# Kernel optimization log

Hardware: AMD Instinct MI355X
Metric: run time of the kernel (lower is better)

## Reference

```python
import jax, jax.numpy as jnp
import numpy as np

B, F, U, V, C = 2048, 128, 1024, 512, 10

def setup_inputs() -> dict:
    key = jax.random.key(0)
    ks = jax.random.split(key, 8)
    s = lambda k, shape, fan: jax.random.normal(k, shape, dtype=jnp.float32) / np.sqrt(fan)
    return {
        "x": jax.random.normal(ks[0], (B, F), dtype=jnp.float32),
        # ExU first layer per feature: input dim 1 -> U units; weight stored pre-exp
        "exu_w": jax.random.normal(ks[1], (F, U), dtype=jnp.float32) * 0.5 + 4.0,
        "exu_b": jax.random.normal(ks[2], (F,), dtype=jnp.float32) * 0.5,
        # hidden dense per feature: U -> V
        "W1": s(ks[3], (F, U, V), U),
        "b1": jnp.zeros((F, V), dtype=jnp.float32),
        # output dense per feature: V -> C
        "W2": s(ks[4], (F, V, C), V),
        "b2": jnp.zeros((F, C), dtype=jnp.float32),
        # global bias over classes
        "b_out": jnp.zeros((C,), dtype=jnp.float32),
    }

def reference(x, exu_w, exu_b, W1, b1, W2, b2, b_out):
    # ExU unit: h = ReLU-1((x - b) * exp(w)); vectorized over all features at once
    # x: [B,F], exu_w/exu_b: [F,U]/[F] -> h: [B,F,U]
    h = jnp.clip((x - exu_b[None, :])[:, :, None] * jnp.exp(exu_w)[None], 0.0, 1.0)
    # grouped hidden GEMM per feature: [B,F,U] x [F,U,V] -> [B,F,V]
    h2 = jax.nn.relu(jnp.einsum('bfu,fuv->bfv', h, W1) + b1[None])
    # grouped output GEMM: [B,F,V] x [F,V,C] -> [B,F,C]
    weights = jnp.einsum('bfv,fvc->bfc', h2, W2) + b2[None]
    # sum feature contributions + bias, softmax over classes (inference, no dropout)
    logits = jnp.sum(weights, axis=1) + b_out
    return jax.nn.softmax(logits, axis=-1)
```

## Files before the change

kernel.cpp:

```cpp
#include <hip/hip_runtime.h>
#include <hip/hip_bf16.h>


#define F_ 128
#define U_ 1024
#define V_ 512
#define C_ 10
#define B_ 2048

#define SAB 72
#define SH2 136

typedef __attribute__((ext_vector_type(8))) short s16x8;
typedef __attribute__((ext_vector_type(4))) float fx4;

__device__ __forceinline__ unsigned bf16bits(float v) {
  unsigned u = __builtin_bit_cast(unsigned, v);
  return (u + 0x7fffu + ((u >> 16) & 1u)) >> 16;
}

__device__ __forceinline__ unsigned packbf16(float lo, float hi) {
#if __has_builtin(__builtin_amdgcn_cvt_pk_bf16_f32)
  typedef __attribute__((ext_vector_type(2))) __bf16 b2t;
  b2t p = __builtin_amdgcn_cvt_pk_bf16_f32(lo, hi);
  return __builtin_bit_cast(unsigned, p);
#else
  return bf16bits(lo) | (bf16bits(hi) << 16);
#endif
}

__global__ void nam_prep(const float* __restrict__ exu_w, const float* __restrict__ b2,
                         const float* __restrict__ b_out,
                         float* __restrict__ emin, float* __restrict__ biasc,
                         int* __restrict__ count, float* __restrict__ logits_mid)
{
  __shared__ float red[256];
  const int bid = blockIdx.x, t = threadIdx.x;
  if (bid < F_) {
    fx4 wv = *(const fx4*)(exu_w + (size_t)bid * U_ + t * 4);
    float m = fminf(fminf(expf(wv.x), expf(wv.y)), fminf(expf(wv.z), expf(wv.w)));
    red[t] = m;
    __syncthreads();
    for (int s = 128; s > 0; s >>= 1) {
      if (t < s) red[t] = fminf(red[t], red[t + s]);
      __syncthreads();
    }
    if (t == 0) emin[bid] = red[0];
  } else if (bid == F_) {
    if (t < C_) {
      float s = b_out[t];
      for (int ff = 0; ff < F_; ++ff) s += b2[ff * C_ + t];
      biasc[t] = s;
    } else if (t >= 32 && t < 32 + F_) {
      count[t - 32] = 0;
    }
  } else {
    const int idx = (bid - F_ - 1) * 256 + t;
    logits_mid[idx] = 0.f;
  }
}

__global__ void nam_classify(const float* __restrict__ x, const float* __restrict__ exu_b,
                             const float* __restrict__ emin,
                             int* __restrict__ count, int* __restrict__ listb)
{
  const int t = threadIdx.x;
  const int f = t & 127, sub = t >> 7;
  const int b = blockIdx.x * 2 + sub;
  const float d = x[(size_t)b * F_ + f] - exu_b[f];
  if (d > 0.f && d * emin[f] < 1.f) {
    const int idx = atomicAdd(count + f, 1);
    listb[f * B_ + idx] = b;
  }
}

__global__ __launch_bounds__(256, 2) void nam_mid(
    const float* __restrict__ x, const float* __restrict__ exu_w,
    const float* __restrict__ exu_b, const float* __restrict__ W1,
    const float* __restrict__ b1, const float* __restrict__ W2,
    const int* __restrict__ listb, const int* __restrict__ count,
    float* __restrict__ colsum1, float* __restrict__ logits_mid)
{
  __shared__ __attribute__((aligned(16))) char smem[49408];
  unsigned short* Alds = (unsigned short*)smem;
  unsigned short* Blds = (unsigned short*)(smem + 18432);
  unsigned short* H2   = (unsigned short*)smem;
  float*          eL   = (float*)(smem + 36864);
  unsigned short* W2T  = (unsigned short*)(smem + 40960);
  float*          rsum = (float*)(smem + 45312);

  const int bx = blockIdx.x;
  const int nb = bx & 3;
  const int f  = bx >> 2;

  const int tid  = threadIdx.x;
  const int l    = tid & 63;
  const int w    = tid >> 6;
  const int wm   = (w >> 1) * 64;
  const int wn   = (w & 1) * 64;
  const int quad = l >> 4;
  const int ln16 = l & 15;

  {
    fx4 wv = *(const fx4*)(exu_w + (size_t)f * U_ + tid * 4);
    fx4 ev;
    ev.x = expf(wv.x); ev.y = expf(wv.y); ev.z = expf(wv.z); ev.w = expf(wv.w);
    *(fx4*)(eL + tid * 4) = ev;
  }
#pragma unroll
  for (int it = 0; it < 8; ++it) {
    const int idx = tid + it * 256;
    const int c = idx & 15, v = idx >> 4;
    float val = (c < C_) ? W2[((size_t)f * V_ + nb * 128 + v) * C_ + c] : 0.f;
    W2T[c * SH2 + v] = (unsigned short)bf16bits(val);
  }

  const int   nmid = count[f];
  const float bfv  = exu_b[f];

  const int mrow = tid >> 4;
  const int lk4  = (tid & 15) * 4;
  const int aswz = (mrow & 7) * 8;

  const int n4  = (tid & 31) * 4;
  const int kb2 = (tid >> 5) * 2;
  const float* w1b = W1 + (size_t)f * U_ * V_ + nb * 128 + n4;

  float csum[4] = {0.f, 0.f, 0.f, 0.f};
  const int nchunk = nmid > 0 ? ((nmid + 127) >> 7) : 1;

  __syncthreads();

  for (int ch = 0; ch < nchunk; ++ch) {
    float d[8];
#pragma unroll
    for (int j = 0; j < 8; ++j) {
      const int gi = ch * 128 + mrow + 16 * j;
      if (gi < nmid) {
        const int bb = listb[f * B_ + gi];
        d[j] = x[(size_t)bb * F_ + f] - bfv;
      } else {
        d[j] = 0.f;
      }
    }

    fx4 acc[4][4];
#pragma unroll
    for (int i = 0; i < 4; ++i)
#pragma unroll
      for (int j = 0; j < 4; ++j)
        acc[i][j] = fx4{0.f, 0.f, 0.f, 0.f};

    for (int kt = 0; kt < 16; ++kt) {
      fx4 ev = *(const fx4*)(eL + kt * 64 + lk4);
#pragma unroll
      for (int j = 0; j < 8; ++j) {
        const int m = mrow + 16 * j;
        float h0 = fminf(fmaxf(d[j] * ev.x, 0.f), 1.f);
        float h1 = fminf(fmaxf(d[j] * ev.y, 0.f), 1.f);
        float h2 = fminf(fmaxf(d[j] * ev.z, 0.f), 1.f);
        float h3 = fminf(fmaxf(d[j] * ev.w, 0.f), 1.f);
        uint2 pk;
        pk.x = packbf16(h0, h1);
        pk.y = packbf16(h2, h3);
        *(uint2*)(Alds + m * SAB + (lk4 ^ aswz)) = pk;
      }
#pragma unroll
      for (int r = 0; r < 4; ++r) {
        const int k0 = kb2 + 16 * r;
        fx4 r0 = *(const fx4*)(w1b + (size_t)(kt * 64 + k0) * V_);
        fx4 r1 = *(const fx4*)(w1b + (size_t)(kt * 64 + k0 + 1) * V_);
        if (ch == 0) {
#pragma unroll
          for (int c = 0; c < 4; ++c) csum[c] += r0[c] + r1[c];
        }
#pragma unroll
        for (int c = 0; c < 4; ++c) {
          const int n = n4 + c;
          unsigned dw = packbf16(r0[c], r1[c]);
          *(unsigned*)(Blds + n * SAB + (k0 ^ (((n >> 2) & 7) * 8))) = dw;
        }
      }
      __syncthreads();

#pragma unroll
      for (int kk = 0; kk < 2; ++kk) {
        const int k0 = kk * 32 + quad * 8;
        s16x8 af[4], bfr[4];
#pragma unroll
        for (int i = 0; i < 4; ++i) {
          const int m = wm + i * 16 + ln16;
          af[i] = *(const s16x8*)(Alds + m * SAB + (k0 ^ ((m & 7) * 8)));
        }
#pragma unroll
        for (int j = 0; j < 4; ++j) {
          const int n = wn + j * 16 + ln16;
          bfr[j] = *(const s16x8*)(Blds + n * SAB + (k0 ^ (((n >> 2) & 7) * 8)));
        }
#pragma unroll
        for (int i = 0; i < 4; ++i)
#pragma unroll
          for (int j = 0; j < 4; ++j)
            acc[i][j] = __builtin_amdgcn_mfma_f32_16x16x32_bf16(af[i], bfr[j], acc[i][j], 0, 0, 0);
      }
      __syncthreads();
    }

    if (ch == 0) {
      rsum[(tid >> 5) * 128 + n4 + 0] = csum[0];
      rsum[(tid >> 5) * 128 + n4 + 1] = csum[1];
      rsum[(tid >> 5) * 128 + n4 + 2] = csum[2];
      rsum[(tid >> 5) * 128 + n4 + 3] = csum[3];
      __syncthreads();
      if (tid < 128) {
        float s = 0.f;
#pragma unroll
        for (int g = 0; g < 8; ++g) s += rsum[g * 128 + tid];
        colsum1[(size_t)f * V_ + nb * 128 + tid] = s;
      }
    }

#pragma unroll
    for (int j = 0; j < 4; ++j) {
      const int n = wn + j * 16 + ln16;
      const float b1v = b1[(size_t)f * V_ + nb * 128 + n];
#pragma unroll
      for (int i = 0; i < 4; ++i)
#pragma unroll
        for (int reg = 0; reg < 4; ++reg) {
          const int m = wm + i * 16 + quad * 4 + reg;
          float v = fmaxf(acc[i][j][reg] + b1v, 0.f);
          H2[m * SH2 + n] = (unsigned short)bf16bits(v);
        }
    }
    __syncthreads();

    fx4 acc2[4];
#pragma unroll
    for (int i = 0; i < 4; ++i) acc2[i] = fx4{0.f, 0.f, 0.f, 0.f};
    const int kj = wn;
#pragma unroll
    for (int kk = 0; kk < 2; ++kk) {
      const int k0 = kj + kk * 32 + quad * 8;
      s16x8 bfr = *(const s16x8*)(W2T + ln16 * SH2 + k0);
#pragma unroll
      for (int i = 0; i < 4; ++i) {
        const int m = wm + i * 16 + ln16;
        s16x8 afr = *(const s16x8*)(H2 + m * SH2 + k0);
        acc2[i] = __builtin_amdgcn_mfma_f32_16x16x32_bf16(afr, bfr, acc2[i], 0, 0, 0);
      }
    }

    if (ln16 < C_) {
#pragma unroll
      for (int i = 0; i < 4; ++i)
#pragma unroll
        for (int reg = 0; reg < 4; ++reg) {
          const int ml = wm + i * 16 + quad * 4 + reg;
          const int gm = ch * 128 + ml;
          if (gm < nmid) {
            const int bb = listb[f * B_ + gm];
            atomicAdd(logits_mid + (size_t)bb * C_ + ln16, acc2[i][reg]);
          }
        }
    }
    __syncthreads();
  }
}

__global__ void nam_tables(const float* __restrict__ colsum1, const float* __restrict__ b1,
                           const float* __restrict__ W2,
                           float* __restrict__ zlog, float* __restrict__ olog)
{
  const int f = blockIdx.x, t = threadIdx.x;
  float a0[C_], a1[C_];
#pragma unroll
  for (int c = 0; c < C_; ++c) { a0[c] = 0.f; a1[c] = 0.f; }
#pragma unroll
  for (int rep = 0; rep < 2; ++rep) {
    const int v = t + rep * 256;
    const float b1v = b1[(size_t)f * V_ + v];
    const float hz = fmaxf(b1v, 0.f);
    const float ho = fmaxf(colsum1[(size_t)f * V_ + v] + b1v, 0.f);
    const float* w2p = W2 + ((size_t)f * V_ + v) * C_;
#pragma unroll
    for (int c = 0; c < C_; ++c) {
      const float wv = w2p[c];
      a0[c] += hz * wv;
      a1[c] += ho * wv;
    }
  }
#pragma unroll
  for (int off = 32; off > 0; off >>= 1)
#pragma unroll
    for (int c = 0; c < C_; ++c) {
      a0[c] += __shfl_down(a0[c], off);
      a1[c] += __shfl_down(a1[c], off);
    }
  __shared__ float red[4][2 * C_];
  const int wv_ = t >> 6, ln = t & 63;
  if (ln == 0)
#pragma unroll
    for (int c = 0; c < C_; ++c) { red[wv_][c] = a0[c]; red[wv_][C_ + c] = a1[c]; }
  __syncthreads();
  if (t < 2 * C_) {
    const float s = red[0][t] + red[1][t] + red[2][t] + red[3][t];
    if (t < C_) zlog[t * F_ + f] = s;
    else        olog[(t - C_) * F_ + f] = s;
  }
}

__global__ void nam_final(const float* __restrict__ x, const float* __restrict__ exu_b,
                          const float* __restrict__ emin,
                          const float* __restrict__ zlog, const float* __restrict__ olog,
                          const float* __restrict__ biasc, const float* __restrict__ logits_mid,
                          float* __restrict__ out)
{
  const int t = threadIdx.x;
  const int f = t & 127, sub = t >> 7;
  const int b = blockIdx.x * 2 + sub;
  const float d  = x[(size_t)b * F_ + f] - exu_b[f];
  const float em = emin[f];
  const bool is_zero = !(d > 0.f);
  const bool is_one  = (d > 0.f) && (d * em >= 1.f);
  float a[C_];
#pragma unroll
  for (int c = 0; c < C_; ++c) {
    const float zv = zlog[c * F_ + f];
    const float ov = olog[c * F_ + f];
    a[c] = is_zero ? zv : (is_one ? ov : 0.f);
  }
#pragma unroll
  for (int off = 32; off > 0; off >>= 1)
#pragma unroll
    for (int c = 0; c < C_; ++c) a[c] += __shfl_down(a[c], off);
  __shared__ float red[4][C_];
  __shared__ float lg[2][C_];
  const int wv_ = t >> 6, ln = t & 63;
  if (ln == 0)
#pragma unroll
    for (int c = 0; c < C_; ++c) red[wv_][c] = a[c];
  __syncthreads();
  if (t < 2 * C_) {
    const int rb = t / C_, c = t % C_;
    lg[rb][c] = red[rb * 2][c] + red[rb * 2 + 1][c]
              + logits_mid[(size_t)(blockIdx.x * 2 + rb) * C_ + c] + biasc[c];
  }
  __syncthreads();
  if (t < 2) {
    float mx = -3.0e38f;
#pragma unroll
    for (int c = 0; c < C_; ++c) mx = fmaxf(mx, lg[t][c]);
    float e[C_];
    float s = 0.f;
#pragma unroll
    for (int c = 0; c < C_; ++c) { e[c] = expf(lg[t][c] - mx); s += e[c]; }
    const float inv = 1.f / s;
#pragma unroll
    for (int c = 0; c < C_; ++c) out[(size_t)(blockIdx.x * 2 + t) * C_ + c] = e[c] * inv;
  }
}

extern "C" void kernel_launch(void* const* d_in, const int* in_sizes, int n_in,
                              void* d_out, int out_size, void* d_ws, size_t ws_size,
                              hipStream_t stream)
{
  const float* x     = (const float*)d_in[0];
  const float* exu_w = (const float*)d_in[1];
  const float* exu_b = (const float*)d_in[2];
  const float* W1    = (const float*)d_in[3];
  const float* b1    = (const float*)d_in[4];
  const float* W2    = (const float*)d_in[5];
  const float* b2    = (const float*)d_in[6];
  const float* b_out = (const float*)d_in[7];
  float* out = (float*)d_out;

  char* ws = (char*)d_ws;
  float* emin       = (float*)(ws + 0);
  float* biasc      = (float*)(ws + 512);
  int*   count      = (int*)  (ws + 576);
  int*   listb      = (int*)  (ws + 1088);
  float* colsum1    = (float*)(ws + 1049664);
  float* zlog       = (float*)(ws + 1311808);
  float* olog       = (float*)(ws + 1316928);
  float* logits_mid = (float*)(ws + 1322048);

  nam_prep<<<F_ + 1 + (B_ * C_ / 256), 256, 0, stream>>>(exu_w, b2, b_out, emin, biasc, count, logits_mid);
  nam_classify<<<B_ / 2, 256, 0, stream>>>(x, exu_b, emin, count, listb);
  nam_mid<<<F_ * 4, 256, 0, stream>>>(x, exu_w, exu_b, W1, b1, W2, listb, count, colsum1, logits_mid);
  nam_tables<<<F_, 256, 0, stream>>>(colsum1, b1, W2, zlog, olog);
  nam_final<<<B_ / 2, 256, 0, stream>>>(x, exu_b, emin, zlog, olog, biasc, logits_mid, out);
}
```

Before: 422.0 us.

## Double-buffer W1 tiles with register prefetch and fold tables kernel into mid

The mid GEMM now uses two LDS buffers for the A and B tiles and prefetches the next W1 tile from global memory into registers while the current tile is being packed and multiplied. This is meant to hide global load latency behind MFMA work. The separate nam_tables kernel is removed; its per-feature zero/one logit tables are computed inside nam_mid and accumulated into zlog/olog with atomics, which nam_prep now zeroes. The prep kernel also takes the min before exp instead of exponentiating every element. LDS use per block rises to about 76KB, which may lower occupancy, and the extra prefetch registers add register pressure.

```diff
diff --git a/kernel.cpp b/kernel.cpp
--- a/kernel.cpp
+++ b/kernel.cpp
@@ -32,20 +32,20 @@
 __global__ void nam_prep(const float* __restrict__ exu_w, const float* __restrict__ b2,
                          const float* __restrict__ b_out,
                          float* __restrict__ emin, float* __restrict__ biasc,
-                         int* __restrict__ count, float* __restrict__ logits_mid)
+                         int* __restrict__ count, float* __restrict__ logits_mid,
+                         float* __restrict__ zlog, float* __restrict__ olog)
 {
   __shared__ float red[256];
   const int bid = blockIdx.x, t = threadIdx.x;
   if (bid < F_) {
     fx4 wv = *(const fx4*)(exu_w + (size_t)bid * U_ + t * 4);
-    float m = fminf(fminf(expf(wv.x), expf(wv.y)), fminf(expf(wv.z), expf(wv.w)));
-    red[t] = m;
+    red[t] = fminf(fminf(wv.x, wv.y), fminf(wv.z, wv.w));
     __syncthreads();
     for (int s = 128; s > 0; s >>= 1) {
       if (t < s) red[t] = fminf(red[t], red[t + s]);
       __syncthreads();
     }
-    if (t == 0) emin[bid] = red[0];
+    if (t == 0) emin[bid] = expf(red[0]);
   } else if (bid == F_) {
     if (t < C_) {
       float s = b_out[t];
@@ -54,6 +54,7 @@
     } else if (t >= 32 && t < 32 + F_) {
       count[t - 32] = 0;
     }
+    for (int i = t; i < C_ * F_; i += 256) { zlog[i] = 0.f; olog[i] = 0.f; }
   } else {
     const int idx = (bid - F_ - 1) * 256 + t;
     logits_mid[idx] = 0.f;
@@ -79,15 +80,19 @@
     const float* __restrict__ exu_b, const float* __restrict__ W1,
     const float* __restrict__ b1, const float* __restrict__ W2,
     const int* __restrict__ listb, const int* __restrict__ count,
-    float* __restrict__ colsum1, float* __restrict__ logits_mid)
+    float* __restrict__ colsum1, float* __restrict__ logits_mid,
+    float* __restrict__ zlog, float* __restrict__ olog)
 {
-  __shared__ __attribute__((aligned(16))) char smem[49408];
-  unsigned short* Alds = (unsigned short*)smem;
-  unsigned short* Blds = (unsigned short*)(smem + 18432);
-  unsigned short* H2   = (unsigned short*)smem;
-  float*          eL   = (float*)(smem + 36864);
-  unsigned short* W2T  = (unsigned short*)(smem + 40960);
-  float*          rsum = (float*)(smem + 45312);
+  __shared__ __attribute__((aligned(16))) char smem[77824];
+  unsigned short* A0  = (unsigned short*)smem;
+  unsigned short* B0  = (unsigned short*)(smem + 18432);
+  unsigned short* A1  = (unsigned short*)(smem + 36864);
+  unsigned short* B1  = (unsigned short*)(smem + 55296);
+  unsigned short* H2  = (unsigned short*)smem;
+  unsigned short* W2T = (unsigned short*)(smem + 36864);
+  float*          rsum= (float*)(smem + 41216);
+  float*          redt= (float*)(smem + 45312);
+  float*          eL  = (float*)(smem + 73728);
 
   const int bx = blockIdx.x;
   const int nb = bx & 3;
@@ -107,13 +112,6 @@
     ev.x = expf(wv.x); ev.y = expf(wv.y); ev.z = expf(wv.z); ev.w = expf(wv.w);
     *(fx4*)(eL + tid * 4) = ev;
   }
-#pragma unroll
-  for (int it = 0; it < 8; ++it) {
-    const int idx = tid + it * 256;
-    const int c = idx & 15, v = idx >> 4;
-    float val = (c < C_) ? W2[((size_t)f * V_ + nb * 128 + v) * C_ + c] : 0.f;
-    W2T[c * SH2 + v] = (unsigned short)bf16bits(val);
-  }
 
   const int   nmid = count[f];
   const float bfv  = exu_b[f];
@@ -122,25 +120,100 @@
   const int lk4  = (tid & 15) * 4;
   const int aswz = (mrow & 7) * 8;
 
-  const int n4  = (tid & 31) * 4;
-  const int kb2 = (tid >> 5) * 2;
+  const int c    = tid & 31;
+  const int n4   = c * 4;
+  const int kq   = tid >> 5;
+  const int bswz = (c & 7) * 8;
   const float* w1b = W1 + (size_t)f * U_ * V_ + nb * 128 + n4;
 
   float csum[4] = {0.f, 0.f, 0.f, 0.f};
   const int nchunk = nmid > 0 ? ((nmid + 127) >> 7) : 1;
 
+  fx4 pre0[8], pre1[8];
+
+#define ISSUE_B(pre, kt)                                                        \
+  {                                                                             \
+    _Pragma("unroll")                                                           \
+    for (int r = 0; r < 2; ++r)                                                 \
+      _Pragma("unroll")                                                         \
+      for (int i = 0; i < 4; ++i)                                               \
+        pre[r * 4 + i] = *(const fx4*)(w1b + (size_t)((kt) * 64 + kq * 4 + r * 32 + i) * V_); \
+  }
+
+#define PACK_B(pre, Bb, do_sum)                                                 \
+  {                                                                             \
+    _Pragma("unroll")                                                           \
+    for (int r = 0; r < 2; ++r) {                                               \
+      const int k0 = kq * 4 + r * 32;                                           \
+      if (do_sum) {                                                             \
+        _Pragma("unroll")                                                       \
+        for (int c2 = 0; c2 < 4; ++c2)                                          \
+          csum[c2] += pre[r*4+0][c2] + pre[r*4+1][c2] + pre[r*4+2][c2] + pre[r*4+3][c2]; \
+      }                                                                         \
+      _Pragma("unroll")                                                         \
+      for (int c2 = 0; c2 < 4; ++c2) {                                          \
+        uint2 pk;                                                               \
+        pk.x = packbf16(pre[r*4+0][c2], pre[r*4+1][c2]);                        \
+        pk.y = packbf16(pre[r*4+2][c2], pre[r*4+3][c2]);                        \
+        *(uint2*)(Bb + (n4 + c2) * SAB + (k0 ^ bswz)) = pk;                     \
+      }                                                                         \
+    }                                                                           \
+  }
+
+#define STAGE_A(kt, Ab)                                                         \
+  {                                                                             \
+    fx4 ev = *(const fx4*)(eL + (kt) * 64 + lk4);                               \
+    _Pragma("unroll")                                                           \
+    for (int j = 0; j < 8; ++j) {                                               \
+      const int m = mrow + 16 * j;                                              \
+      float h0 = fminf(fmaxf(d[j] * ev.x, 0.f), 1.f);                           \
+      float h1 = fminf(fmaxf(d[j] * ev.y, 0.f), 1.f);                           \
+      float h2 = fminf(fmaxf(d[j] * ev.z, 0.f), 1.f);                           \
+      float h3 = fminf(fmaxf(d[j] * ev.w, 0.f), 1.f);                           \
+      uint2 pk;                                                                 \
+      pk.x = packbf16(h0, h1);                                                  \
+      pk.y = packbf16(h2, h3);                                                  \
+      *(uint2*)(Ab + m * SAB + (lk4 ^ aswz)) = pk;                              \
+    }                                                                           \
+  }
+
+#define MFMA_STEP(Ab, Bb)                                                       \
+  {                                                                             \
+    _Pragma("unroll")                                                           \
+    for (int kk = 0; kk < 2; ++kk) {                                            \
+      const int k0 = kk * 32 + quad * 8;                                        \
+      s16x8 af[4], bfr[4];                                                      \
+      _Pragma("unroll")                                                         \
+      for (int i = 0; i < 4; ++i) {                                             \
+        const int m = wm + i * 16 + ln16;                                       \
+        af[i] = *(const s16x8*)(Ab + m * SAB + (k0 ^ ((m & 7) * 8)));           \
+      }                                                                         \
+      _Pragma("unroll")                                                         \
+      for (int j = 0; j < 4; ++j) {                                             \
+        const int n = wn + j * 16 + ln16;                                       \
+        bfr[j] = *(const s16x8*)(Bb + n * SAB + (k0 ^ (((n >> 2) & 7) * 8)));   \
+      }                                                                         \
+      _Pragma("unroll")                                                         \
+      for (int i = 0; i < 4; ++i)                                               \
+        _Pragma("unroll")                                                       \
+        for (int j = 0; j < 4; ++j)                                             \
+          acc[i][j] = __builtin_amdgcn_mfma_f32_16x16x32_bf16(af[i], bfr[j], acc[i][j], 0, 0, 0); \
+    }                                                                           \
+  }
+
+  ISSUE_B(pre0, 0);
   __syncthreads();
 
   for (int ch = 0; ch < nchunk; ++ch) {
+    const bool do_sum = (ch == 0);
     float d[8];
 #pragma unroll
     for (int j = 0; j < 8; ++j) {
       const int gi = ch * 128 + mrow + 16 * j;
+      d[j] = 0.f;
       if (gi < nmid) {
         const int bb = listb[f * B_ + gi];
         d[j] = x[(size_t)bb * F_ + f] - bfv;
-      } else {
-        d[j] = 0.f;
       }
     }
 
@@ -151,73 +224,19 @@
       for (int j = 0; j < 4; ++j)
         acc[i][j] = fx4{0.f, 0.f, 0.f, 0.f};
 
-    for (int kt = 0; kt < 16; ++kt) {
-      fx4 ev = *(const fx4*)(eL + kt * 64 + lk4);
-#pragma unroll
-      for (int j = 0; j < 8; ++j) {
-        const int m = mrow + 16 * j;
-        float h0 = fminf(fmaxf(d[j] * ev.x, 0.f), 1.f);
-        float h1 = fminf(fmaxf(d[j] * ev.y, 0.f), 1.f);
-        float h2 = fminf(fmaxf(d[j] * ev.z, 0.f), 1.f);
-        float h3 = fminf(fmaxf(d[j] * ev.w, 0.f), 1.f);
-        uint2 pk;
-        pk.x = packbf16(h0, h1);
-        pk.y = packbf16(h2, h3);
-        *(uint2*)(Alds + m * SAB + (lk4 ^ aswz)) = pk;
-      }
-#pragma unroll
-      for (int r = 0; r < 4; ++r) {
-        const int k0 = kb2 + 16 * r;
-        fx4 r0 = *(const fx4*)(w1b + (size_t)(kt * 64 + k0) * V_);
-        fx4 r1 = *(const fx4*)(w1b + (size_t)(kt * 64 + k0 + 1) * V_);
-        if (ch == 0) {
-#pragma unroll
-          for (int c = 0; c < 4; ++c) csum[c] += r0[c] + r1[c];
-        }
-#pragma unroll
-        for (int c = 0; c < 4; ++c) {
-          const int n = n4 + c;
-          unsigned dw = packbf16(r0[c], r1[c]);
-          *(unsigned*)(Blds + n * SAB + (k0 ^ (((n >> 2) & 7) * 8))) = dw;
-        }
-      }
+    for (int kt2 = 0; kt2 < 8; ++kt2) {
+      const int kt = kt2 * 2;
+      STAGE_A(kt, A0);
+      PACK_B(pre0, B0, do_sum);
+      ISSUE_B(pre1, kt + 1);
       __syncthreads();
-
-#pragma unroll
-      for (int kk = 0; kk < 2; ++kk) {
-        const int k0 = kk * 32 + quad * 8;
-        s16x8 af[4], bfr[4];
-#pragma unroll
-        for (int i = 0; i < 4; ++i) {
-          const int m = wm + i * 16 + ln16;
-          af[i] = *(const s16x8*)(Alds + m * SAB + (k0 ^ ((m & 7) * 8)));
-        }
-#pragma unroll
-        for (int j = 0; j < 4; ++j) {
-          const int n = wn + j * 16 + ln16;
-          bfr[j] = *(const s16x8*)(Blds + n * SAB + (k0 ^ (((n >> 2) & 7) * 8)));
-        }
-#pragma unroll
-        for (int i = 0; i < 4; ++i)
-#pragma unroll
-          for (int j = 0; j < 4; ++j)
-            acc[i][j] = __builtin_amdgcn_mfma_f32_16x16x32_bf16(af[i], bfr[j], acc[i][j], 0, 0, 0);
-      }
+      MFMA_STEP(A0, B0);
+      STAGE_A(kt + 1, A1);
+      PACK_B(pre1, B1, do_sum);
+      if (kt2 < 7) { ISSUE_B(pre0, kt + 2); }
+      else if (ch + 1 < nchunk) { ISSUE_B(pre0, 0); }
       __syncthreads();
-    }
-
-    if (ch == 0) {
-      rsum[(tid >> 5) * 128 + n4 + 0] = csum[0];
-      rsum[(tid >> 5) * 128 + n4 + 1] = csum[1];
-      rsum[(tid >> 5) * 128 + n4 + 2] = csum[2];
-      rsum[(tid >> 5) * 128 + n4 + 3] = csum[3];
-      __syncthreads();
-      if (tid < 128) {
-        float s = 0.f;
-#pragma unroll
-        for (int g = 0; g < 8; ++g) s += rsum[g * 128 + tid];
-        colsum1[(size_t)f * V_ + nb * 128 + tid] = s;
-      }
+      MFMA_STEP(A1, B1);
     }
 
 #pragma unroll
@@ -235,19 +254,67 @@
     }
     __syncthreads();
 
+#pragma unroll
+    for (int it = 0; it < 8; ++it) {
+      const int idx = tid + it * 256;
+      const int cc = idx & 15, v = idx >> 4;
+      float val = (cc < C_) ? W2[((size_t)f * V_ + nb * 128 + v) * C_ + cc] : 0.f;
+      W2T[cc * SH2 + v] = (unsigned short)bf16bits(val);
+    }
+    if (do_sum) {
+      rsum[kq * 128 + n4 + 0] = csum[0];
+      rsum[kq * 128 + n4 + 1] = csum[1];
+      rsum[kq * 128 + n4 + 2] = csum[2];
+      rsum[kq * 128 + n4 + 3] = csum[3];
+    }
+    __syncthreads();
+
     fx4 acc2[4];
 #pragma unroll
     for (int i = 0; i < 4; ++i) acc2[i] = fx4{0.f, 0.f, 0.f, 0.f};
-    const int kj = wn;
 #pragma unroll
     for (int kk = 0; kk < 2; ++kk) {
-      const int k0 = kj + kk * 32 + quad * 8;
+      const int k0 = wn + kk * 32 + quad * 8;
       s16x8 bfr = *(const s16x8*)(W2T + ln16 * SH2 + k0);
 #pragma unroll
       for (int i = 0; i < 4; ++i) {
         const int m = wm + i * 16 + ln16;
         s16x8 afr = *(const s16x8*)(H2 + m * SH2 + k0);
         acc2[i] = __builtin_amdgcn_mfma_f32_16x16x32_bf16(afr, bfr, acc2[i], 0, 0, 0);
+      }
+    }
+
+    if (do_sum && tid < 128) {
+      float s = 0.f;
+#pragma unroll
+      for (int g = 0; g < 8; ++g) s += rsum[g * 128 + tid];
+      const int v = nb * 128 + tid;
+      colsum1[(size_t)f * V_ + v] = s;
+      const float b1v = b1[(size_t)f * V_ + v];
+      const float hz = fmaxf(b1v, 0.f);
+      const float ho = fmaxf(s + b1v, 0.f);
+      const float* w2p = W2 + ((size_t)f * V_ + v) * C_;
+      float a0[C_], a1[C_];
+#pragma unroll
+      for (int cc = 0; cc < C_; ++cc) {
+        const float wv = w2p[cc];
+        a0[cc] = hz * wv;
+        a1[cc] = ho * wv;
+      }
+#pragma unroll
+      for (int off = 32; off > 0; off >>= 1)
+#pragma unroll
+        for (int cc = 0; cc < C_; ++cc) {
+          a0[cc] += __shfl_down(a0[cc], off);
+          a1[cc] += __shfl_down(a1[cc], off);
+        }
+      if ((tid & 63) == 0) {
+        const int wv_ = tid >> 6;
+#pragma unroll
+        for (int cc = 0; cc < C_; ++cc) {
+          redt[wv_ * 20 + cc] = a0[cc];
+          redt[wv_ * 20 + C_ + cc] = a1[cc];
+        }
       }
     }
 
@@ -265,49 +332,17 @@
         }
     }
     __syncthreads();
-  }
-}
-
-__global__ void nam_tables(const float* __restrict__ colsum1, const float* __restrict__ b1,
-                           const float* __restrict__ W2,
-                           float* __restrict__ zlog, float* __restrict__ olog)
-{
-  const int f = blockIdx.x, t = threadIdx.x;
-  float a0[C_], a1[C_];
-#pragma unroll
-  for (int c = 0; c < C_; ++c) { a0[c] = 0.f; a1[c] = 0.f; }
-#pragma unroll
-  for (int rep = 0; rep < 2; ++rep) {
-    const int v = t + rep * 256;
-    const float b1v = b1[(size_t)f * V_ + v];
-    const float hz = fmaxf(b1v, 0.f);
-    const float ho = fmaxf(colsum1[(size_t)f * V_ + v] + b1v, 0.f);
-    const float* w2p = W2 + ((size_t)f * V_ + v) * C_;
-#pragma unroll
-    for (int c = 0; c < C_; ++c) {
-      const float wv = w2p[c];
-      a0[c] += hz * wv;
-      a1[c] += ho * wv;
-    }
-  }
-#pragma unroll
-  for (int off = 32; off > 0; off >>= 1)
-#pragma unroll
-    for (int c = 0; c < C_; ++c) {
-      a0[c] += __shfl_down(a0[c], off);
-      a1[c] += __shfl_down(a1[c], off);
-    }
-  __shared__ float red[4][2 * C_];
-  const int wv_ = t >> 6, ln = t & 63;
-  if (ln == 0)
-#pragma unroll
-    for (int c = 0; c < C_; ++c) { red[wv_][c] = a0[c]; red[wv_][C_ + c] = a1[c]; }
-  __syncthreads();
-  if (t < 2 * C_) {
-    const float s = red[0][t] + red[1][t] + red[2][t] + red[3][t];
-    if (t < C_) zlog[t * F_ + f] = s;
-    else        olog[(t - C_) * F_ + f] = s;
-  }
+
+    if (do_sum && tid < 20) {
+      const float sv = redt[tid] + redt[20 + tid];
+      if (tid < C_) atomicAdd(zlog + tid * F_ + f, sv);
+      else          atomicAdd(olog + (tid - C_) * F_ + f, sv);
+    }
+  }
+#undef ISSUE_B
+#undef PACK_B
+#undef STAGE_A
+#undef MFMA_STEP
 }
 
 __global__ void nam_final(const float* __restrict__ x, const float* __restrict__ exu_b,
@@ -385,9 +420,10 @@
   float* olog       = (float*)(ws + 1316928);
   float* logits_mid = (float*)(ws + 1322048);
 
-  nam_prep<<<F_ + 1 + (B_ * C_ / 256), 256, 0, stream>>>(exu_w, b2, b_out, emin, biasc, count, logits_mid);
+  nam_prep<<<F_ + 1 + (B_ * C_ / 256), 256, 0, stream>>>(exu_w, b2, b_out, emin, biasc,
+                                                          count, logits_mid, zlog, olog);
   nam_classify<<<B_ / 2, 256, 0, stream>>>(x, exu_b, emin, count, listb);
-  nam_mid<<<F_ * 4, 256, 0, stream>>>(x, exu_w, exu_b, W1, b1, W2, listb, count, colsum1, logits_mid);
-  nam_tables<<<F_, 256, 0, stream>>>(colsum1, b1, W2, zlog, olog);
+  nam_mid<<<F_ * 4, 256, 0, stream>>>(x, exu_w, exu_b, W1, b1, W2, listb, count,
+                                       colsum1, logits_mid, zlog, olog);
   nam_final<<<B_ / 2, 256, 0, stream>>>(x, exu_b, emin, zlog, olog, biasc, logits_mid, out);
 }
```

After: 416.0 us. Within noise of the previous version (-1.4%).

## Replace per-feature mid GEMM with sorted-threshold prefix sums over W1

Applied to the files above, without the earlier changes.

Sorts exp(exu_w) per feature and, for each batch element in the non-saturated range, finds its clip threshold by binary search. A single streaming pass over W1 in sorted order then accumulates prefix sums S=Σe·w and T=Σw, so each hidden pre-activation is d·S−T plus the saturated column sum, with no GEMM and no bf16 rounding. This cuts the work from a B×U×V matmul to one read of W1 plus per-row outputs. In exchange it adds bitonic sorts, gathered W1 row reads, a large intermediate buffer and a separate small output-layer kernel.

```diff
diff --git a/kernel.cpp b/kernel.cpp
--- a/kernel.cpp
+++ b/kernel.cpp
@@ -1,5 +1,4 @@
 #include <hip/hip_runtime.h>
-#include <hip/hip_bf16.h>
 
 
 #define F_ 128
@@ -7,45 +6,36 @@
 #define V_ 512
 #define C_ 10
 #define B_ 2048
-
-#define SAB 72
-#define SH2 136
-
-typedef __attribute__((ext_vector_type(8))) short s16x8;
-typedef __attribute__((ext_vector_type(4))) float fx4;
-
-__device__ __forceinline__ unsigned bf16bits(float v) {
-  unsigned u = __builtin_bit_cast(unsigned, v);
-  return (u + 0x7fffu + ((u >> 16) & 1u)) >> 16;
-}
-
-__device__ __forceinline__ unsigned packbf16(float lo, float hi) {
-#if __has_builtin(__builtin_amdgcn_cvt_pk_bf16_f32)
-  typedef __attribute__((ext_vector_type(2))) __bf16 b2t;
-  b2t p = __builtin_amdgcn_cvt_pk_bf16_f32(lo, hi);
-  return __builtin_bit_cast(unsigned, p);
-#else
-  return bf16bits(lo) | (bf16bits(hi) << 16);
-#endif
-}
-
-__global__ void nam_prep(const float* __restrict__ exu_w, const float* __restrict__ b2,
+#define UN 16
+
+__global__ void nam_sort(const float* __restrict__ exu_w, const float* __restrict__ b2,
                          const float* __restrict__ b_out,
+                         unsigned long long* __restrict__ skeys_g,
                          float* __restrict__ emin, float* __restrict__ biasc,
                          int* __restrict__ count, float* __restrict__ logits_mid)
 {
-  __shared__ float red[256];
   const int bid = blockIdx.x, t = threadIdx.x;
   if (bid < F_) {
-    fx4 wv = *(const fx4*)(exu_w + (size_t)bid * U_ + t * 4);
-    float m = fminf(fminf(expf(wv.x), expf(wv.y)), fminf(expf(wv.z), expf(wv.w)));
-    red[t] = m;
+    __shared__ unsigned long long keys[1024];
+    for (int i = t; i < U_; i += 256) {
+      float e = expf(exu_w[(size_t)bid * U_ + i]);
+      keys[i] = ((unsigned long long)__builtin_bit_cast(unsigned, e) << 32) | (unsigned)i;
+    }
     __syncthreads();
-    for (int s = 128; s > 0; s >>= 1) {
-      if (t < s) red[t] = fminf(red[t], red[t + s]);
-      __syncthreads();
-    }
-    if (t == 0) emin[bid] = red[0];
+    for (int k = 2; k <= 1024; k <<= 1)
+      for (int j = k >> 1; j > 0; j >>= 1) {
+        for (int i = t; i < 1024; i += 256) {
+          const int p = i ^ j;
+          if (p > i) {
+            unsigned long long a = keys[i], b = keys[p];
+            const bool up = ((i & k) == 0);
+            if (up ? (a > b) : (a < b)) { keys[i] = b; keys[p] = a; }
+          }
+        }
+        __syncthreads();
+      }
+    for (int i = t; i < 1024; i += 256) skeys_g[(size_t)bid * U_ + i] = keys[i];
+    if (t == 0) emin[bid] = __builtin_bit_cast(float, (unsigned)(keys[0] >> 32));
   } else if (bid == F_) {
     if (t < C_) {
       float s = b_out[t];
@@ -74,197 +64,158 @@
   }
 }
 
-__global__ __launch_bounds__(256, 2) void nam_mid(
-    const float* __restrict__ x, const float* __restrict__ exu_w,
-    const float* __restrict__ exu_b, const float* __restrict__ W1,
-    const float* __restrict__ b1, const float* __restrict__ W2,
+__global__ __launch_bounds__(128) void nam_stream(
+    const float* __restrict__ x, const float* __restrict__ exu_b,
+    const float* __restrict__ W1,
+    const unsigned long long* __restrict__ skeys_g,
     const int* __restrict__ listb, const int* __restrict__ count,
-    float* __restrict__ colsum1, float* __restrict__ logits_mid)
-{
-  __shared__ __attribute__((aligned(16))) char smem[49408];
-  unsigned short* Alds = (unsigned short*)smem;
-  unsigned short* Blds = (unsigned short*)(smem + 18432);
-  unsigned short* H2   = (unsigned short*)smem;
-  float*          eL   = (float*)(smem + 36864);
-  unsigned short* W2T  = (unsigned short*)(smem + 40960);
-  float*          rsum = (float*)(smem + 45312);
-
-  const int bx = blockIdx.x;
-  const int nb = bx & 3;
-  const int f  = bx >> 2;
-
+    float* __restrict__ colsum1, float* __restrict__ h2pre,
+    int* __restrict__ bout)
+{
+  __shared__ unsigned long long skeys[1024];
+  __shared__ unsigned pkey[2048];
+  __shared__ float    darr[2048];
+  __shared__ int      barr[2048];
+
+  const int bx   = blockIdx.x;
+  const int f    = bx >> 1;
+  const int half = bx & 1;
   const int tid  = threadIdx.x;
-  const int l    = tid & 63;
-  const int w    = tid >> 6;
-  const int wm   = (w >> 1) * 64;
-  const int wn   = (w & 1) * 64;
-  const int quad = l >> 4;
-  const int ln16 = l & 15;
-
-  {
-    fx4 wv = *(const fx4*)(exu_w + (size_t)f * U_ + tid * 4);
-    fx4 ev;
-    ev.x = expf(wv.x); ev.y = expf(wv.y); ev.z = expf(wv.z); ev.w = expf(wv.w);
-    *(fx4*)(eL + tid * 4) = ev;
-  }
-#pragma unroll
-  for (int it = 0; it < 8; ++it) {
-    const int idx = tid + it * 256;
-    const int c = idx & 15, v = idx >> 4;
-    float val = (c < C_) ? W2[((size_t)f * V_ + nb * 128 + v) * C_ + c] : 0.f;
-    W2T[c * SH2 + v] = (unsigned short)bf16bits(val);
-  }
-
-  const int   nmid = count[f];
-  const float bfv  = exu_b[f];
-
-  const int mrow = tid >> 4;
-  const int lk4  = (tid & 15) * 4;
-  const int aswz = (mrow & 7) * 8;
-
-  const int n4  = (tid & 31) * 4;
-  const int kb2 = (tid >> 5) * 2;
-  const float* w1b = W1 + (size_t)f * U_ * V_ + nb * 128 + n4;
-
-  float csum[4] = {0.f, 0.f, 0.f, 0.f};
-  const int nchunk = nmid > 0 ? ((nmid + 127) >> 7) : 1;
-
-  __syncthreads();
-
-  for (int ch = 0; ch < nchunk; ++ch) {
-    float d[8];
-#pragma unroll
-    for (int j = 0; j < 8; ++j) {
-      const int gi = ch * 128 + mrow + 16 * j;
-      if (gi < nmid) {
-        const int bb = listb[f * B_ + gi];
-        d[j] = x[(size_t)bb * F_ + f] - bfv;
-      } else {
-        d[j] = 0.f;
-      }
-    }
-
-    fx4 acc[4][4];
-#pragma unroll
-    for (int i = 0; i < 4; ++i)
-#pragma unroll
-      for (int j = 0; j < 4; ++j)
-        acc[i][j] = fx4{0.f, 0.f, 0.f, 0.f};
-
-    for (int kt = 0; kt < 16; ++kt) {
-      fx4 ev = *(const fx4*)(eL + kt * 64 + lk4);
-#pragma unroll
-      for (int j = 0; j < 8; ++j) {
-        const int m = mrow + 16 * j;
-        float h0 = fminf(fmaxf(d[j] * ev.x, 0.f), 1.f);
-        float h1 = fminf(fmaxf(d[j] * ev.y, 0.f), 1.f);
-        float h2 = fminf(fmaxf(d[j] * ev.z, 0.f), 1.f);
-        float h3 = fminf(fmaxf(d[j] * ev.w, 0.f), 1.f);
-        uint2 pk;
-        pk.x = packbf16(h0, h1);
-        pk.y = packbf16(h2, h3);
-        *(uint2*)(Alds + m * SAB + (lk4 ^ aswz)) = pk;
-      }
-#pragma unroll
-      for (int r = 0; r < 4; ++r) {
-        const int k0 = kb2 + 16 * r;
-        fx4 r0 = *(const fx4*)(w1b + (size_t)(kt * 64 + k0) * V_);
-        fx4 r1 = *(const fx4*)(w1b + (size_t)(kt * 64 + k0 + 1) * V_);
-        if (ch == 0) {
-#pragma unroll
-          for (int c = 0; c < 4; ++c) csum[c] += r0[c] + r1[c];
-        }
-#pragma unroll
-        for (int c = 0; c < 4; ++c) {
-          const int n = n4 + c;
-          unsigned dw = packbf16(r0[c], r1[c]);
-          *(unsigned*)(Blds + n * SAB + (k0 ^ (((n >> 2) & 7) * 8))) = dw;
-        }
-      }
-      __syncthreads();
-
-#pragma unroll
-      for (int kk = 0; kk < 2; ++kk) {
-        const int k0 = kk * 32 + quad * 8;
-        s16x8 af[4], bfr[4];
-#pragma unroll
-        for (int i = 0; i < 4; ++i) {
-          const int m = wm + i * 16 + ln16;
-          af[i] = *(const s16x8*)(Alds + m * SAB + (k0 ^ ((m & 7) * 8)));
-        }
-#pragma unroll
-        for (int j = 0; j < 4; ++j) {
-          const int n = wn + j * 16 + ln16;
-          bfr[j] = *(const s16x8*)(Blds + n * SAB + (k0 ^ (((n >> 2) & 7) * 8)));
-        }
-#pragma unroll
-        for (int i = 0; i < 4; ++i)
-#pragma unroll
-          for (int j = 0; j < 4; ++j)
-            acc[i][j] = __builtin_amdgcn_mfma_f32_16x16x32_bf16(af[i], bfr[j], acc[i][j], 0, 0, 0);
-      }
-      __syncthreads();
-    }
-
-    if (ch == 0) {
-      rsum[(tid >> 5) * 128 + n4 + 0] = csum[0];
-      rsum[(tid >> 5) * 128 + n4 + 1] = csum[1];
-      rsum[(tid >> 5) * 128 + n4 + 2] = csum[2];
-      rsum[(tid >> 5) * 128 + n4 + 3] = csum[3];
-      __syncthreads();
-      if (tid < 128) {
-        float s = 0.f;
-#pragma unroll
-        for (int g = 0; g < 8; ++g) s += rsum[g * 128 + tid];
-        colsum1[(size_t)f * V_ + nb * 128 + tid] = s;
-      }
-    }
-
-#pragma unroll
-    for (int j = 0; j < 4; ++j) {
-      const int n = wn + j * 16 + ln16;
-      const float b1v = b1[(size_t)f * V_ + nb * 128 + n];
-#pragma unroll
-      for (int i = 0; i < 4; ++i)
-#pragma unroll
-        for (int reg = 0; reg < 4; ++reg) {
-          const int m = wm + i * 16 + quad * 4 + reg;
-          float v = fmaxf(acc[i][j][reg] + b1v, 0.f);
-          H2[m * SH2 + n] = (unsigned short)bf16bits(v);
-        }
-    }
-    __syncthreads();
-
-    fx4 acc2[4];
-#pragma unroll
-    for (int i = 0; i < 4; ++i) acc2[i] = fx4{0.f, 0.f, 0.f, 0.f};
-    const int kj = wn;
-#pragma unroll
-    for (int kk = 0; kk < 2; ++kk) {
-      const int k0 = kj + kk * 32 + quad * 8;
-      s16x8 bfr = *(const s16x8*)(W2T + ln16 * SH2 + k0);
-#pragma unroll
-      for (int i = 0; i < 4; ++i) {
-        const int m = wm + i * 16 + ln16;
-        s16x8 afr = *(const s16x8*)(H2 + m * SH2 + k0);
-        acc2[i] = __builtin_amdgcn_mfma_f32_16x16x32_bf16(afr, bfr, acc2[i], 0, 0, 0);
-      }
-    }
-
-    if (ln16 < C_) {
-#pragma unroll
-      for (int i = 0; i < 4; ++i)
-#pragma unroll
-        for (int reg = 0; reg < 4; ++reg) {
-          const int ml = wm + i * 16 + quad * 4 + reg;
-          const int gm = ch * 128 + ml;
-          if (gm < nmid) {
-            const int bb = listb[f * B_ + gm];
-            atomicAdd(logits_mid + (size_t)bb * C_ + ln16, acc2[i][reg]);
+
+  for (int i = tid; i < 1024; i += 128) skeys[i] = skeys_g[(size_t)f * U_ + i];
+  const int nmid = count[f];
+  const float bfv = exu_b[f];
+  __syncthreads();
+
+  for (int i = tid; i < nmid; i += 128) {
+    const int b = listb[f * B_ + i];
+    const float d = x[(size_t)b * F_ + f] - bfv;
+    darr[i] = d;
+    barr[i] = b;
+    const float thr = 1.0f / d;
+    int lo = 0, hi = 1024;
+#pragma unroll
+    for (int s = 0; s < 10; ++s) {
+      const int mid = (lo + hi) >> 1;
+      const float e = __builtin_bit_cast(float, (unsigned)(skeys[mid] >> 32));
+      if (e < thr) lo = mid + 1; else hi = mid;
+      if (lo >= hi) {  }
+    }
+    pkey[i] = ((unsigned)lo << 11) | (unsigned)i;
+  }
+  int npow2 = 2;
+  while (npow2 < nmid) npow2 <<= 1;
+  for (int i = tid; i < npow2; i += 128)
+    if (i >= nmid) pkey[i] = 0xFFFFFFFFu;
+  __syncthreads();
+  if (nmid > 1) {
+    for (int k = 2; k <= npow2; k <<= 1)
+      for (int j = k >> 1; j > 0; j >>= 1) {
+        for (int i = tid; i < npow2; i += 128) {
+          const int p = i ^ j;
+          if (p > i) {
+            unsigned a = pkey[i], b = pkey[p];
+            const bool up = ((i & k) == 0);
+            if (up ? (a > b) : (a < b)) { pkey[i] = b; pkey[p] = a; }
           }
         }
-    }
-    __syncthreads();
+        __syncthreads();
+      }
+  }
+
+  const float* Wf = W1 + (size_t)f * (U_ * V_) + half * 256 + 2 * tid;
+  typedef __attribute__((ext_vector_type(2))) float f2;
+  f2 cur[UN], nxt[UN];
+  float ecur[UN], enxt[UN];
+#pragma unroll
+  for (int q = 0; q < UN; ++q) {
+    const unsigned long long kk = skeys[q];
+    cur[q] = *(const f2*)(Wf + ((unsigned)(kk & 1023u) << 9));
+    ecur[q] = __builtin_bit_cast(float, (unsigned)(kk >> 32));
+  }
+  float S0 = 0.f, S1 = 0.f, T0 = 0.f, T1 = 0.f;
+  int pp = 0;
+  int next_r = (nmid > 0) ? (int)(pkey[0] >> 11) : 99999;
+
+  for (int blk = 0; blk < 1024 / UN; ++blk) {
+    if (blk < 1024 / UN - 1) {
+#pragma unroll
+      for (int q = 0; q < UN; ++q) {
+        const unsigned long long kk = skeys[(blk + 1) * UN + q];
+        nxt[q] = *(const f2*)(Wf + ((unsigned)(kk & 1023u) << 9));
+        enxt[q] = __builtin_bit_cast(float, (unsigned)(kk >> 32));
+      }
+    }
+#pragma unroll
+    for (int q = 0; q < UN; ++q) {
+      const int i = blk * UN + q;
+      while (pp < nmid && next_r <= i) {
+        const unsigned pk = pkey[pp];
+        const int idx = (int)(pk & 2047u);
+        const float dd = darr[idx];
+        f2 outv;
+        outv.x = dd * S0 - T0;
+        outv.y = dd * S1 - T1;
+        *(f2*)(h2pre + ((size_t)f * B_ + pp) * V_ + half * 256 + 2 * tid) = outv;
+        if (tid == 0 && half == 0) bout[f * B_ + pp] = barr[idx];
+        ++pp;
+        next_r = (pp < nmid) ? (int)(pkey[pp] >> 11) : 99999;
+      }
+      const float e = ecur[q];
+      const f2 wv = cur[q];
+      S0 = fmaf(e, wv.x, S0);
+      S1 = fmaf(e, wv.y, S1);
+      T0 += wv.x;
+      T1 += wv.y;
+    }
+#pragma unroll
+    for (int q = 0; q < UN; ++q) { cur[q] = nxt[q]; ecur[q] = enxt[q]; }
+  }
+  while (pp < nmid) {
+    const unsigned pk = pkey[pp];
+    const int idx = (int)(pk & 2047u);
+    const float dd = darr[idx];
+    f2 outv;
+    outv.x = dd * S0 - T0;
+    outv.y = dd * S1 - T1;
+    *(f2*)(h2pre + ((size_t)f * B_ + pp) * V_ + half * 256 + 2 * tid) = outv;
+    if (tid == 0 && half == 0) bout[f * B_ + pp] = barr[idx];
+    ++pp;
+  }
+  f2 cs; cs.x = T0; cs.y = T1;
+  *(f2*)(colsum1 + f * V_ + half * 256 + 2 * tid) = cs;
+}
+
+__global__ void nam_fin_mid(const int* __restrict__ count, const int* __restrict__ bout,
+                            const float* __restrict__ h2pre, const float* __restrict__ colsum1,
+                            const float* __restrict__ b1, const float* __restrict__ W2,
+                            float* __restrict__ logits_mid)
+{
+  const int f = blockIdx.x, t = threadIdx.x;
+  const int wave = t >> 6, lane = t & 63;
+  const int nmid = count[f];
+  for (int row = wave; row < nmid; row += 4) {
+    const int b = bout[f * B_ + row];
+    const float* pre = h2pre + ((size_t)f * B_ + row) * V_ + lane * 8;
+    const float* csp = colsum1 + f * V_ + lane * 8;
+    const float* b1p = b1 + (size_t)f * V_ + lane * 8;
+    float acc[C_];
+#pragma unroll
+    for (int c = 0; c < C_; ++c) acc[c] = 0.f;
+#pragma unroll
+    for (int j = 0; j < 8; ++j) {
+      const float h = fmaxf(pre[j] + csp[j] + b1p[j], 0.f);
+      const float* w2p = W2 + ((size_t)f * V_ + lane * 8 + j) * C_;
+#pragma unroll
+      for (int c = 0; c < C_; ++c) acc[c] = fmaf(h, w2p[c], acc[c]);
+    }
+#pragma unroll
+    for (int off = 32; off > 0; off >>= 1)
+#pragma unroll
+      for (int c = 0; c < C_; ++c) acc[c] += __shfl_down(acc[c], off);
+    if (lane == 0)
+#pragma unroll
+      for (int c = 0; c < C_; ++c) atomicAdd(logits_mid + (size_t)b * C_ + c, acc[c]);
   }
 }
 
@@ -384,10 +335,16 @@
   float* zlog       = (float*)(ws + 1311808);
   float* olog       = (float*)(ws + 1316928);
   float* logits_mid = (float*)(ws + 1322048);
-
-  nam_prep<<<F_ + 1 + (B_ * C_ / 256), 256, 0, stream>>>(exu_w, b2, b_out, emin, biasc, count, logits_mid);
+  unsigned long long* skeys_g = (unsigned long long*)(ws + 1404928);
+  int*   bout       = (int*)  (ws + 2453504);
+  float* h2pre      = (float*)(ws + 4194304);
+
+  nam_sort<<<F_ + 1 + (B_ * C_ / 256), 256, 0, stream>>>(exu_w, b2, b_out, skeys_g,
+                                                          emin, biasc, count, logits_mid);
   nam_classify<<<B_ / 2, 256, 0, stream>>>(x, exu_b, emin, count, listb);
-  nam_mid<<<F_ * 4, 256, 0, stream>>>(x, exu_w, exu_b, W1, b1, W2, listb, count, colsum1, logits_mid);
+  nam_stream<<<F_ * 2, 128, 0, stream>>>(x, exu_b, W1, skeys_g, listb, count,
+                                          colsum1, h2pre, bout);
+  nam_fin_mid<<<F_, 256, 0, stream>>>(count, bout, h2pre, colsum1, b1, W2, logits_mid);
   nam_tables<<<F_, 256, 0, stream>>>(colsum1, b1, W2, zlog, olog);
   nam_final<<<B_ / 2, 256, 0, stream>>>(x, exu_b, emin, zlog, olog, biasc, logits_mid, out);
 }
```

Result: slower. 515.7 us (+22.2%).
